# Performance work log

Hardware: AMD Instinct MI355X
Metric: run time of the kernel (lower is better)

## Reference

```python
import jax, jax.numpy as jnp
import numpy as np

LEAK = 0.2  # LeakyReLU alpha

def setup_inputs() -> dict:
    key = jax.random.key(0)
    k1, k2, k3, k4 = jax.random.split(key, 4)
    B, N, D, H = 4, 1024, 64, 64
    qs = jax.random.normal(k1, (B, N, D), dtype=jnp.float32)
    ks = jax.random.normal(k2, (B, N, D), dtype=jnp.float32)
    vs = jax.random.normal(k3, (B, N, D), dtype=jnp.float32)
    W = jax.random.normal(k4, (3 * D, H), dtype=jnp.float32) * 0.05  # Dense kernel on concat(q,k,q-k)
    b = jnp.zeros((H,), dtype=jnp.float32)
    a = jnp.ones((H,), dtype=jnp.float32)
    return {"qs": qs, "ks": ks, "vs": vs, "W": W, "b": b, "a": a}

def reference(qs, ks, vs, W, b, a):
    D = qs.shape[-1]
    norm = 1.0 / jnp.sqrt(jnp.asarray(D, dtype=qs.dtype))
    # Dense on concat(q, k, q-k) splits as q@(Wq+Wd) + k@(Wk-Wd) + b,
    # avoiding the O(N^2 * 3D) concat tensor (same math as TF concat->Dense).
    Wq, Wk, Wd = W[:D], W[D:2 * D], W[2 * D:]
    hq = qs @ (Wq + Wd)            # [B, N, H]  query-side term
    hk = ks @ (Wk - Wd)            # [B, N, H]  key-side term
    h = hq[:, :, None, :] + hk[:, None, :, :] + b   # [B, N, N, H]
    h = jnp.where(h > 0, h, LEAK * h)               # LeakyReLU(0.2)
    scores = jnp.einsum('bijh,h->bij', h, a) * norm # [B, N, N]
    att = jax.nn.softmax(scores, axis=-1)
    return jnp.matmul(att, vs)                      # [B, N, D]
```

## Files before the change

kernel.cpp:

```cpp
#include <hip/hip_runtime.h>
#include <math.h>

#define LOG2E 1.4426950408889634f
typedef __attribute__((ext_vector_type(2))) _Float16 h2v;
typedef __attribute__((ext_vector_type(8))) _Float16 f16x8;
typedef __attribute__((ext_vector_type(4))) float f32x4;

static __device__ __forceinline__ unsigned pkrtz_u32(float lo, float hi) {
  auto p = __builtin_amdgcn_cvt_pkrtz(lo, hi);
  unsigned u; __builtin_memcpy(&u, &p, 4); return u;
}
static __device__ __forceinline__ h2v habs2(h2v x) {
  unsigned u; __builtin_memcpy(&u, &x, 4);
  u &= 0x7FFF7FFFu;
  h2v r; __builtin_memcpy(&r, &u, 4); return r;
}
static __device__ __forceinline__ h2v u2h(unsigned u) {
  h2v r; __builtin_memcpy(&r, &u, 4); return r;
}


__global__ __launch_bounds__(256) void prep_kernel(
    const float* __restrict__ qs, const float* __restrict__ ks,
    const float* __restrict__ vs,
    const float* __restrict__ W, const float* __restrict__ bias,
    const float* __restrict__ a,
    unsigned* __restrict__ hq2, uint4* __restrict__ khT4,
    float* __restrict__ Dj, unsigned* __restrict__ abd2,
    uint4* __restrict__ vfrag) {
  __shared__ __align__(16) float wcomb[64][68];
  __shared__ __align__(16) float xin[64][68];
  const int blk = blockIdx.x;
  const int t = threadIdx.x;

  if (blk >= 128) {
    const int unit = blk - 128;
    const int b = unit >> 5, kstep = unit & 31;
    const int lane = t & 63, ntile = t >> 6;
    const int j0 = kstep * 32 + (lane >> 4) * 8;
    const int d = ntile * 16 + (lane & 15);
    const float* vb = vs + b * 1024 * 64;
    unsigned pr[4];
#pragma unroll
    for (int i = 0; i < 4; ++i)
      pr[i] = pkrtz_u32(vb[(j0 + 2 * i) * 64 + d], vb[(j0 + 2 * i + 1) * 64 + d]);
    vfrag[((b * 32 + kstep) * 4 + ntile) * 64 + lane] =
        make_uint4(pr[0], pr[1], pr[2], pr[3]);
    return;
  }

  const bool qpart = blk < 64;
  const int r0 = (qpart ? blk : blk - 64) * 64;
  const float* src = qpart ? qs : ks;
  if (blk == 0 && t < 32)
    abd2[t] = pkrtz_u32(0.05f * a[2 * t], 0.05f * a[2 * t + 1]);
  for (int rep = 0; rep < 16; ++rep) {
    int e = rep * 256 + t;
    int row = e >> 6, col = e & 63;
    float wd = W[(128 + row) * 64 + col];
    float wm = qpart ? (W[row * 64 + col] + wd)
                     : (W[(64 + row) * 64 + col] - wd);
    wcomb[row][col] = wm;
    xin[row][col] = src[(r0 + row) * 64 + col];
  }
  __syncthreads();
  const int r = t >> 2;
  const int h0 = (t & 3) << 4;
  float acc[16];
#pragma unroll
  for (int k = 0; k < 16; ++k) acc[k] = 0.f;
#pragma unroll 8
  for (int d = 0; d < 64; ++d) {
    float xv = xin[r][d];
#pragma unroll
    for (int c = 0; c < 4; ++c) {
      float4 w4 = *(const float4*)&wcomb[d][h0 + (c << 2)];
      acc[c * 4 + 0] = fmaf(xv, w4.x, acc[c * 4 + 0]);
      acc[c * 4 + 1] = fmaf(xv, w4.y, acc[c * 4 + 1]);
      acc[c * 4 + 2] = fmaf(xv, w4.z, acc[c * 4 + 2]);
      acc[c * 4 + 3] = fmaf(xv, w4.w, acc[c * 4 + 3]);
    }
  }
  int grow = r0 + r;
  if (qpart) {
    unsigned pr[8];
#pragma unroll
    for (int i = 0; i < 8; ++i) pr[i] = pkrtz_u32(acc[2 * i], acc[2 * i + 1]);
    uint4* dst = (uint4*)&hq2[grow * 32 + (t & 3) * 8];
    dst[0] = make_uint4(pr[0], pr[1], pr[2], pr[3]);
    dst[1] = make_uint4(pr[4], pr[5], pr[6], pr[7]);
  } else {
    int bidx = grow >> 10;
    int j = grow & 1023;
    float val[16];
    float part = 0.f;
#pragma unroll
    for (int k = 0; k < 16; ++k) {
      val[k] = acc[k] + bias[h0 + k];
      part += a[h0 + k] * val[k];
    }
    part += __shfl_xor(part, 1);
    part += __shfl_xor(part, 2);
    if ((t & 3) == 0) Dj[bidx * 1024 + j] = 0.075f * part;
    unsigned pr[8];
#pragma unroll
    for (int i = 0; i < 8; ++i) pr[i] = pkrtz_u32(val[2 * i], val[2 * i + 1]);
    const int h4a = (t & 3) * 2;
    khT4[(bidx * 8 + h4a) * 1024 + j]     = make_uint4(pr[0], pr[1], pr[2], pr[3]);
    khT4[(bidx * 8 + h4a + 1) * 1024 + j] = make_uint4(pr[4], pr[5], pr[6], pr[7]);
  }
}

__global__ __launch_bounds__(512) void attn14_kernel(
    const uint4* __restrict__ vfrag,
    const unsigned* __restrict__ hq2, const uint4* __restrict__ khT4,
    const float* __restrict__ Dj, const unsigned* __restrict__ abd2,
    float* __restrict__ out) {
  __shared__ __align__(16) unsigned p2u[8 * 520];
  __shared__ __align__(16) float ob[64 * 64];
  __shared__ __align__(16) unsigned q2lds[8 * 32];
  __shared__ __align__(16) unsigned ab2lds[32];
  __shared__ float redm[8][8];
  __shared__ float redl[8][8];

  const int t = threadIdx.x;
  const int lane = t & 63;
  const int w = t >> 6;
  const int b = blockIdx.y;
  const int rowbase = blockIdx.x * 8;
  const int growbase = b * 1024 + rowbase;

  const uint4* kh_b = khT4 + (size_t)b * 8 * 1024;
  const uint4* vf_b = vfrag + (size_t)b * 32 * 4 * 64;

  if (t < 256) q2lds[t] = hq2[growbase * 32 + t];
  if (t >= 256 && t < 288) ab2lds[t - 256] = abd2[t - 256];
  __syncthreads();

  const int jloc = w * 128 + lane * 2;
  float2 d2 = *(const float2*)(Dj + b * 1024 + jloc);

  float s[8][2];
#pragma unroll
  for (int r = 0; r < 8; ++r) { s[r][0] = 0.f; s[r][1] = 0.f; }

  uint4 kc0 = kh_b[jloc], kc1 = kh_b[jloc + 1];
#pragma unroll 1
  for (int it = 0; it < 8; ++it) {
    const int nx = (it < 7) ? it + 1 : it;
    uint4 kn0 = kh_b[nx * 1024 + jloc];
    uint4 kn1 = kh_b[nx * 1024 + jloc + 1];
    uint4 abq = *(const uint4*)&ab2lds[it * 4];
    const unsigned abu[4] = {abq.x, abq.y, abq.z, abq.w};
    const unsigned kcu[2][4] = {{kc0.x, kc0.y, kc0.z, kc0.w},
                                {kc1.x, kc1.y, kc1.z, kc1.w}};
#pragma unroll
    for (int r = 0; r < 8; ++r) {
      uint4 qq = *(const uint4*)&q2lds[r * 32 + it * 4];
      const unsigned qu[4] = {qq.x, qq.y, qq.z, qq.w};
#pragma unroll
      for (int u = 0; u < 4; ++u) {
        h2v qh = u2h(qu[u]);
        h2v a2 = u2h(abu[u]);
        h2v x0 = habs2(qh + u2h(kcu[0][u]));
        s[r][0] = __builtin_amdgcn_fdot2(a2, x0, s[r][0], false);
        h2v x1 = habs2(qh + u2h(kcu[1][u]));
        s[r][1] = __builtin_amdgcn_fdot2(a2, x1, s[r][1], false);
      }
    }
    kc0 = kn0; kc1 = kn1;
  }
#pragma unroll
  for (int r = 0; r < 8; ++r) { s[r][0] += d2.x; s[r][1] += d2.y; }

#pragma unroll
  for (int r = 0; r < 8; ++r) {
    float m = fmaxf(s[r][0], s[r][1]);
#pragma unroll
    for (int off = 32; off >= 1; off >>= 1) m = fmaxf(m, __shfl_xor(m, off));
    if (lane == 0) redm[r][w] = m;
  }
  __syncthreads();
  float mx[8];
#pragma unroll
  for (int r = 0; r < 8; ++r) {
    float4 a0 = *(const float4*)&redm[r][0];
    float4 a1 = *(const float4*)&redm[r][4];
    mx[r] = fmaxf(fmaxf(fmaxf(a0.x, a0.y), fmaxf(a0.z, a0.w)),
                  fmaxf(fmaxf(a1.x, a1.y), fmaxf(a1.z, a1.w)));
  }
#pragma unroll
  for (int r = 0; r < 8; ++r) {
    float p0 = __builtin_amdgcn_exp2f((s[r][0] - mx[r]) * LOG2E);
    float p1 = __builtin_amdgcn_exp2f((s[r][1] - mx[r]) * LOG2E);
    p2u[r * 520 + (jloc >> 1)] = pkrtz_u32(p0, p1);
    float ps = p0 + p1;
#pragma unroll
    for (int off = 32; off >= 1; off >>= 1) ps += __shfl_xor(ps, off);
    if (lane == 0) redl[r][w] = ps;
  }
  __syncthreads();

  f32x4 acc[4];
#pragma unroll
  for (int nt = 0; nt < 4; ++nt) acc[nt] = (f32x4){0.f, 0.f, 0.f, 0.f};
  const int arow = (lane & 7) * 520;
  const int kgr = (lane >> 4) * 8;
#pragma unroll 2
  for (int ks = 0; ks < 4; ++ks) {
    const int j0 = w * 128 + ks * 32;
    uint4 au = *(const uint4*)&p2u[arow + ((j0 + kgr) >> 1)];
    f16x8 af; __builtin_memcpy(&af, &au, 16);
    const int gks = j0 >> 5;
#pragma unroll
    for (int nt = 0; nt < 4; ++nt) {
      uint4 bu = vf_b[(gks * 4 + nt) * 64 + lane];
      f16x8 bf; __builtin_memcpy(&bf, &bu, 16);
      acc[nt] = __builtin_amdgcn_mfma_f32_16x16x32_f16(af, bf, acc[nt], 0, 0, 0);
    }
  }

  if (lane < 32) {
    const int rbase = (lane >> 4) * 4;
#pragma unroll
    for (int nt = 0; nt < 4; ++nt)
#pragma unroll
      for (int rg = 0; rg < 4; ++rg)
        ob[(w * 8 + rbase + rg) * 64 + nt * 16 + (lane & 15)] = acc[nt][rg];
  }
  __syncthreads();
  {
    int r = t >> 6, d = t & 63;
    float ax = 0.f;
#pragma unroll
    for (int wv = 0; wv < 8; ++wv) ax += ob[(wv * 8 + r) * 64 + d];
    float4 l0 = *(const float4*)&redl[r][0];
    float4 l1 = *(const float4*)&redl[r][4];
    float lt = ((l0.x + l0.y) + (l0.z + l0.w)) + ((l1.x + l1.y) + (l1.z + l1.w));
    out[(growbase + r) * 64 + d] = ax / lt;
  }
}

extern "C" void kernel_launch(void* const* d_in, const int* in_sizes, int n_in,
                              void* d_out, int out_size, void* d_ws, size_t ws_size,
                              hipStream_t stream) {
  const float* qs = (const float*)d_in[0];
  const float* ks = (const float*)d_in[1];
  const float* vs = (const float*)d_in[2];
  const float* W  = (const float*)d_in[3];
  const float* bi = (const float*)d_in[4];
  const float* a  = (const float*)d_in[5];
  float* out = (float*)d_out;
  unsigned* hq2   = (unsigned*)d_ws;
  uint4*    khT4  = (uint4*)((char*)d_ws + 524288);
  float*    Dj    = (float*)((char*)d_ws + 1048576);
  unsigned* abd2  = (unsigned*)((char*)d_ws + 1064960);
  uint4*    vfrag = (uint4*)((char*)d_ws + 1065216);
  prep_kernel<<<256, 256, 0, stream>>>(qs, ks, vs, W, bi, a, hq2, khT4, Dj,
                                       abd2, vfrag);
  attn14_kernel<<<dim3(128, 4), 512, 0, stream>>>(vfrag, hq2, khT4, Dj, abd2, out);
}
```

Baseline: 36.30 us.

## Use per-wave local softmax max with deferred rescale and MFMA row-sum

Each wave now computes its own per-row max, packed as fp16 pairs, exponentiates against that local max, and runs the P·V MFMA immediately without a block-wide barrier. The global max is combined afterwards and each wave's partial output is rescaled. The row sum of P comes from an extra ones-column MFMA tile appended to the V fragments, which removes the shuffle sum reduction. The q operand and the a vector are now read straight from global memory in a transposed layout instead of being staged in LDS, dropping the initial barrier. The cost is one extra MFMA tile per step and fp16 precision for the max values.

Measured after the change: 34.05 us. -6.2%, faster.

```diff
diff --git a/kernel.cpp b/kernel.cpp
--- a/kernel.cpp
+++ b/kernel.cpp
@@ -17,6 +17,14 @@
 }
 static __device__ __forceinline__ h2v u2h(unsigned u) {
   h2v r; __builtin_memcpy(&r, &u, 4); return r;
+}
+static __device__ __forceinline__ unsigned pkmax_u(unsigned a, unsigned b) {
+  h2v r = __builtin_elementwise_max(u2h(a), u2h(b));
+  unsigned u; __builtin_memcpy(&u, &r, 4); return u;
+}
+static __device__ __forceinline__ float h2f(unsigned u, int idx) {
+  h2v v = u2h(u);
+  return (float)v[idx];
 }
 
 
@@ -25,7 +33,7 @@
     const float* __restrict__ vs,
     const float* __restrict__ W, const float* __restrict__ bias,
     const float* __restrict__ a,
-    unsigned* __restrict__ hq2, uint4* __restrict__ khT4,
+    unsigned* __restrict__ hq2t, uint4* __restrict__ khT4,
     float* __restrict__ Dj, unsigned* __restrict__ abd2,
     uint4* __restrict__ vfrag) {
   __shared__ __align__(16) float wcomb[64][68];
@@ -44,8 +52,12 @@
 #pragma unroll
     for (int i = 0; i < 4; ++i)
       pr[i] = pkrtz_u32(vb[(j0 + 2 * i) * 64 + d], vb[(j0 + 2 * i + 1) * 64 + d]);
-    vfrag[((b * 32 + kstep) * 4 + ntile) * 64 + lane] =
+    vfrag[((b * 32 + kstep) * 5 + ntile) * 64 + lane] =
         make_uint4(pr[0], pr[1], pr[2], pr[3]);
+    if (t < 64) {
+      unsigned v = ((t & 15) == 0) ? 0x3C003C00u : 0u;
+      vfrag[((b * 32 + kstep) * 5 + 4) * 64 + t] = make_uint4(v, v, v, v);
+    }
     return;
   }
 
@@ -86,9 +98,10 @@
     unsigned pr[8];
 #pragma unroll
     for (int i = 0; i < 8; ++i) pr[i] = pkrtz_u32(acc[2 * i], acc[2 * i + 1]);
-    uint4* dst = (uint4*)&hq2[grow * 32 + (t & 3) * 8];
-    dst[0] = make_uint4(pr[0], pr[1], pr[2], pr[3]);
-    dst[1] = make_uint4(pr[4], pr[5], pr[6], pr[7]);
+    const int base = (grow >> 3) * 256 + (grow & 7) * 4;
+    const int it0 = (t & 3) * 2;
+    *(uint4*)&hq2t[base + it0 * 32]       = make_uint4(pr[0], pr[1], pr[2], pr[3]);
+    *(uint4*)&hq2t[base + (it0 + 1) * 32] = make_uint4(pr[4], pr[5], pr[6], pr[7]);
   } else {
     int bidx = grow >> 10;
     int j = grow & 1023;
@@ -111,17 +124,15 @@
   }
 }
 
-__global__ __launch_bounds__(512) void attn14_kernel(
+__global__ __launch_bounds__(512) void attn15_kernel(
     const uint4* __restrict__ vfrag,
-    const unsigned* __restrict__ hq2, const uint4* __restrict__ khT4,
+    const unsigned* __restrict__ hq2t, const uint4* __restrict__ khT4,
     const float* __restrict__ Dj, const unsigned* __restrict__ abd2,
     float* __restrict__ out) {
   __shared__ __align__(16) unsigned p2u[8 * 520];
   __shared__ __align__(16) float ob[64 * 64];
-  __shared__ __align__(16) unsigned q2lds[8 * 32];
-  __shared__ __align__(16) unsigned ab2lds[32];
-  __shared__ float redm[8][8];
-  __shared__ float redl[8][8];
+  __shared__ __align__(16) unsigned redmu[8 * 4];
+  __shared__ __align__(16) float redl[8 * 8];
 
   const int t = threadIdx.x;
   const int lane = t & 63;
@@ -131,11 +142,8 @@
   const int growbase = b * 1024 + rowbase;
 
   const uint4* kh_b = khT4 + (size_t)b * 8 * 1024;
-  const uint4* vf_b = vfrag + (size_t)b * 32 * 4 * 64;
-
-  if (t < 256) q2lds[t] = hq2[growbase * 32 + t];
-  if (t >= 256 && t < 288) ab2lds[t - 256] = abd2[t - 256];
-  __syncthreads();
+  const uint4* vf_b = vfrag + (size_t)b * 32 * 5 * 64;
+  const unsigned* qt = hq2t + (size_t)growbase * 32;
 
   const int jloc = w * 128 + lane * 2;
   float2 d2 = *(const float2*)(Dj + b * 1024 + jloc);
@@ -150,13 +158,13 @@
     const int nx = (it < 7) ? it + 1 : it;
     uint4 kn0 = kh_b[nx * 1024 + jloc];
     uint4 kn1 = kh_b[nx * 1024 + jloc + 1];
-    uint4 abq = *(const uint4*)&ab2lds[it * 4];
+    uint4 abq = *(const uint4*)(abd2 + it * 4);
     const unsigned abu[4] = {abq.x, abq.y, abq.z, abq.w};
     const unsigned kcu[2][4] = {{kc0.x, kc0.y, kc0.z, kc0.w},
                                 {kc1.x, kc1.y, kc1.z, kc1.w}};
 #pragma unroll
     for (int r = 0; r < 8; ++r) {
-      uint4 qq = *(const uint4*)&q2lds[r * 32 + it * 4];
+      uint4 qq = *(const uint4*)(qt + it * 32 + r * 4);
       const unsigned qu[4] = {qq.x, qq.y, qq.z, qq.w};
 #pragma unroll
       for (int u = 0; u < 4; ++u) {
@@ -173,37 +181,30 @@
 #pragma unroll
   for (int r = 0; r < 8; ++r) { s[r][0] += d2.x; s[r][1] += d2.y; }
 
+  unsigned mp[4];
+#pragma unroll
+  for (int k = 0; k < 4; ++k)
+    mp[k] = pkrtz_u32(fmaxf(s[2 * k][0], s[2 * k][1]),
+                      fmaxf(s[2 * k + 1][0], s[2 * k + 1][1]));
+#pragma unroll
+  for (int off = 32; off >= 1; off >>= 1) {
+#pragma unroll
+    for (int k = 0; k < 4; ++k) mp[k] = pkmax_u(mp[k], __shfl_xor(mp[k], off));
+  }
+  if (lane == 0)
+    *(uint4*)&redmu[w * 4] = make_uint4(mp[0], mp[1], mp[2], mp[3]);
+
 #pragma unroll
   for (int r = 0; r < 8; ++r) {
-    float m = fmaxf(s[r][0], s[r][1]);
-#pragma unroll
-    for (int off = 32; off >= 1; off >>= 1) m = fmaxf(m, __shfl_xor(m, off));
-    if (lane == 0) redm[r][w] = m;
-  }
-  __syncthreads();
-  float mx[8];
-#pragma unroll
-  for (int r = 0; r < 8; ++r) {
-    float4 a0 = *(const float4*)&redm[r][0];
-    float4 a1 = *(const float4*)&redm[r][4];
-    mx[r] = fmaxf(fmaxf(fmaxf(a0.x, a0.y), fmaxf(a0.z, a0.w)),
-                  fmaxf(fmaxf(a1.x, a1.y), fmaxf(a1.z, a1.w)));
-  }
-#pragma unroll
-  for (int r = 0; r < 8; ++r) {
-    float p0 = __builtin_amdgcn_exp2f((s[r][0] - mx[r]) * LOG2E);
-    float p1 = __builtin_amdgcn_exp2f((s[r][1] - mx[r]) * LOG2E);
-    p2u[r * 520 + (jloc >> 1)] = pkrtz_u32(p0, p1);
-    float ps = p0 + p1;
-#pragma unroll
-    for (int off = 32; off >= 1; off >>= 1) ps += __shfl_xor(ps, off);
-    if (lane == 0) redl[r][w] = ps;
-  }
-  __syncthreads();
-
-  f32x4 acc[4];
-#pragma unroll
-  for (int nt = 0; nt < 4; ++nt) acc[nt] = (f32x4){0.f, 0.f, 0.f, 0.f};
+    float mwr = h2f(mp[r >> 1], r & 1);
+    float p0 = __builtin_amdgcn_exp2f((s[r][0] - mwr) * LOG2E);
+    float p1 = __builtin_amdgcn_exp2f((s[r][1] - mwr) * LOG2E);
+    p2u[r * 520 + w * 64 + lane] = pkrtz_u32(p0, p1);
+  }
+
+  f32x4 acc[5];
+#pragma unroll
+  for (int nt = 0; nt < 5; ++nt) acc[nt] = (f32x4){0.f, 0.f, 0.f, 0.f};
   const int arow = (lane & 7) * 520;
   const int kgr = (lane >> 4) * 8;
 #pragma unroll 2
@@ -213,30 +214,58 @@
     f16x8 af; __builtin_memcpy(&af, &au, 16);
     const int gks = j0 >> 5;
 #pragma unroll
-    for (int nt = 0; nt < 4; ++nt) {
-      uint4 bu = vf_b[(gks * 4 + nt) * 64 + lane];
+    for (int nt = 0; nt < 5; ++nt) {
+      uint4 bu = vf_b[(gks * 5 + nt) * 64 + lane];
       f16x8 bf; __builtin_memcpy(&bf, &bu, 16);
       acc[nt] = __builtin_amdgcn_mfma_f32_16x16x32_f16(af, bf, acc[nt], 0, 0, 0);
     }
   }
+  __syncthreads();
+
+  unsigned Mp[4];
+  {
+    uint4 v0 = *(const uint4*)&redmu[0];
+    Mp[0] = v0.x; Mp[1] = v0.y; Mp[2] = v0.z; Mp[3] = v0.w;
+#pragma unroll
+    for (int wv = 1; wv < 8; ++wv) {
+      uint4 vv = *(const uint4*)&redmu[wv * 4];
+      Mp[0] = pkmax_u(Mp[0], vv.x); Mp[1] = pkmax_u(Mp[1], vv.y);
+      Mp[2] = pkmax_u(Mp[2], vv.z); Mp[3] = pkmax_u(Mp[3], vv.w);
+    }
+  }
+  const int rb = ((lane >> 4) & 1) * 4;
+  float sc[4];
+#pragma unroll
+  for (int rg = 0; rg < 4; ++rg) {
+    int r = rb + rg;
+    float mwv = h2f(mp[r >> 1], r & 1);
+    float Mv = h2f(Mp[r >> 1], r & 1);
+    sc[rg] = __builtin_amdgcn_exp2f((mwv - Mv) * LOG2E);
+  }
 
   if (lane < 32) {
-    const int rbase = (lane >> 4) * 4;
 #pragma unroll
     for (int nt = 0; nt < 4; ++nt)
 #pragma unroll
       for (int rg = 0; rg < 4; ++rg)
-        ob[(w * 8 + rbase + rg) * 64 + nt * 16 + (lane & 15)] = acc[nt][rg];
+        ob[(w * 8 + rb + rg) * 64 + nt * 16 + (lane & 15)] = acc[nt][rg] * sc[rg];
+  }
+  if ((lane & 47) == 0) {
+    float4 lv;
+    lv.x = acc[4][0] * sc[0]; lv.y = acc[4][1] * sc[1];
+    lv.z = acc[4][2] * sc[2]; lv.w = acc[4][3] * sc[3];
+    *(float4*)&redl[w * 8 + rb] = lv;
   }
   __syncthreads();
+
   {
     int r = t >> 6, d = t & 63;
-    float ax = 0.f;
-#pragma unroll
-    for (int wv = 0; wv < 8; ++wv) ax += ob[(wv * 8 + r) * 64 + d];
-    float4 l0 = *(const float4*)&redl[r][0];
-    float4 l1 = *(const float4*)&redl[r][4];
-    float lt = ((l0.x + l0.y) + (l0.z + l0.w)) + ((l1.x + l1.y) + (l1.z + l1.w));
+    float ax = 0.f, lt = 0.f;
+#pragma unroll
+    for (int wv = 0; wv < 8; ++wv) {
+      ax += ob[(wv * 8 + r) * 64 + d];
+      lt += redl[wv * 8 + r];
+    }
     out[(growbase + r) * 64 + d] = ax / lt;
   }
 }
@@ -251,12 +280,12 @@
   const float* bi = (const float*)d_in[4];
   const float* a  = (const float*)d_in[5];
   float* out = (float*)d_out;
-  unsigned* hq2   = (unsigned*)d_ws;
+  unsigned* hq2t  = (unsigned*)d_ws;
   uint4*    khT4  = (uint4*)((char*)d_ws + 524288);
   float*    Dj    = (float*)((char*)d_ws + 1048576);
   unsigned* abd2  = (unsigned*)((char*)d_ws + 1064960);
   uint4*    vfrag = (uint4*)((char*)d_ws + 1065216);
-  prep_kernel<<<256, 256, 0, stream>>>(qs, ks, vs, W, bi, a, hq2, khT4, Dj,
+  prep_kernel<<<256, 256, 0, stream>>>(qs, ks, vs, W, bi, a, hq2t, khT4, Dj,
                                        abd2, vfrag);
-  attn14_kernel<<<dim3(128, 4), 512, 0, stream>>>(vfrag, hq2, khT4, Dj, abd2, out);
-}
+  attn15_kernel<<<dim3(128, 4), 512, 0, stream>>>(vfrag, hq2t, khT4, Dj, abd2, out);
+}
```
